# Kernel tuning notes

Hardware: AMD Instinct MI355X
Metric: run time of the kernel (lower is better)

## Reference

```python
import jax, jax.numpy as jnp
import numpy as np

B, D, R, E = 16384, 512, 64, 8

def setup_inputs() -> dict:
    key = jax.random.key(0)
    ks = jax.random.split(key, 8)
    return {
        "x0": jax.random.normal(ks[0], (B, D), jnp.float32),
        "x": jax.random.normal(ks[1], (B, D), jnp.float32),
        "U": jax.random.normal(ks[2], (E, D, R), jnp.float32) * 0.02,
        "V": jax.random.normal(ks[3], (E, R, D), jnp.float32) * 0.02,
        "C": jax.random.normal(ks[4], (E, R, R), jnp.float32) * 0.02,
        "b": jnp.zeros((E, D), jnp.float32),
        "Wg": jax.random.normal(ks[5], (E, D), jnp.float32) * 0.02,
        "bg": jnp.zeros((E,), jnp.float32),
    }

def reference(x0, x, U, V, C, b, Wg, bg):
    # gate: softmax over experts
    g = jax.nn.softmax(x @ Wg.T + bg, axis=1)            # [B, E]
    # per-expert low-rank bilinear transform, batched over experts
    xv = jnp.einsum('bd,erd->ber', x, V)                 # x @ V[e].T
    xvc = jnp.einsum('ber,ers->bes', xv, C)              # xv @ C[e]
    proj = jnp.einsum('bes,eds->bed', xvc, U)            # xvc @ U[e].T
    # gated sum: sum_e g_e * (x0*proj_e + b_e + x)
    gproj = jnp.einsum('be,bed->bd', g, proj)
    out = x0 * gproj + g @ b + x * g.sum(axis=1, keepdims=True)
    return out
```

## Files before the change

### kernel.cpp

```cpp
#include <hip/hip_runtime.h>
#include <math.h>


typedef __bf16 bf16_t;
typedef __attribute__((ext_vector_type(8))) __bf16 bf16x8;
typedef __attribute__((ext_vector_type(4))) __bf16 bf16x4;
typedef __attribute__((ext_vector_type(4))) float  floatx4;

__global__ __launch_bounds__(256) void prep_kernel(
    const float* __restrict__ U, const float* __restrict__ V, const float* __restrict__ C,
    bf16_t* __restrict__ VCc, bf16_t* __restrict__ Ut) {
  int tid = blockIdx.x * 256 + threadIdx.x;
  if (tid < 512 * 512) {
    int n = tid >> 9, d = tid & 511;
    int e = n >> 6, s = n & 63;
    const float* Vp = V + (size_t)e * 64 * 512 + d;
    const float* Cp = C + (size_t)e * 64 * 64 + s;
    float acc = 0.f;
#pragma unroll 8
    for (int r = 0; r < 64; ++r) acc += Vp[(size_t)r * 512] * Cp[r * 64];
    VCc[tid] = (bf16_t)acc;
  } else {
    int i2 = tid - 512 * 512;
    int d = i2 >> 9, n = i2 & 511;
    int e = n >> 6, s = n & 63;
    Ut[i2] = (bf16_t)U[((size_t)e * 512 + d) * 64 + s];
  }
}

__global__ __launch_bounds__(256) void gate_kernel(
    const float* __restrict__ x, const float* __restrict__ Wg, const float* __restrict__ bg,
    bf16_t* __restrict__ xbf, float* __restrict__ g) {
  int wave = threadIdx.x >> 6, lane = threadIdx.x & 63;
  int row = blockIdx.x * 4 + wave;
  const float4* xr = (const float4*)(x + (size_t)row * 512);
  float4 v0 = xr[lane];
  float4 v1 = xr[lane + 64];
  bf16x4* xb = (bf16x4*)(xbf + (size_t)row * 512);
  bf16x4 b0, b1;
  b0.x = (bf16_t)v0.x; b0.y = (bf16_t)v0.y; b0.z = (bf16_t)v0.z; b0.w = (bf16_t)v0.w;
  b1.x = (bf16_t)v1.x; b1.y = (bf16_t)v1.y; b1.z = (bf16_t)v1.z; b1.w = (bf16_t)v1.w;
  xb[lane] = b0;
  xb[lane + 64] = b1;
  float acc[8];
#pragma unroll
  for (int e = 0; e < 8; ++e) {
    const float4* wp = (const float4*)(Wg + (size_t)e * 512);
    float4 w0 = wp[lane], w1 = wp[lane + 64];
    acc[e] = v0.x * w0.x + v0.y * w0.y + v0.z * w0.z + v0.w * w0.w +
             v1.x * w1.x + v1.y * w1.y + v1.z * w1.z + v1.w * w1.w;
  }
#pragma unroll
  for (int e = 0; e < 8; ++e) {
#pragma unroll
    for (int off = 32; off > 0; off >>= 1) acc[e] += __shfl_xor(acc[e], off, 64);
  }
  float z[8], mx = -1e30f;
#pragma unroll
  for (int e = 0; e < 8; ++e) { z[e] = acc[e] + bg[e]; mx = fmaxf(mx, z[e]); }
  float s = 0.f;
#pragma unroll
  for (int e = 0; e < 8; ++e) { z[e] = __expf(z[e] - mx); s += z[e]; }
  float inv = 1.f / s;
  if (lane == 0) {
#pragma unroll
    for (int e = 0; e < 8; ++e) g[(size_t)row * 8 + e] = z[e] * inv;
  }
}

__device__ __forceinline__ void gemm_stream(
    const bf16_t* __restrict__ A, const bf16_t* __restrict__ Bt,
    char* ldsB, int m0, int n0, int t, floatx4 acc[2][4]) {
  {
    const float4* src = (const float4*)(Bt + (size_t)n0 * 512);
#pragma unroll
    for (int i = 0; i < 16; ++i) {
      int G = i * 256 + t;
      int n = G >> 6, c = G & 63;
      *(float4*)(ldsB + n * 1024 + ((c ^ (n & 7)) << 4)) = src[G];
    }
  }
  __syncthreads();
  const int lane = t & 63, wave = t >> 6;
  const int lhi = lane >> 4, llo = lane & 15;
  const char* pA0 = (const char*)A + (size_t)(m0 + wave * 32 + llo) * 1024 + lhi * 16;
  const char* pA1 = pA0 + 16 * 1024;
  const char* pB = ldsB + llo * 1024;
  const int bsw = (llo & 7) << 4;
#pragma unroll 4
  for (int ks = 0; ks < 16; ++ks) {
    bf16x8 a0 = *(const bf16x8*)(pA0 + ks * 64);
    bf16x8 a1 = *(const bf16x8*)(pA1 + ks * 64);
    bf16x8 bf[4];
#pragma unroll
    for (int nf = 0; nf < 4; ++nf)
      bf[nf] = *(const bf16x8*)(pB + nf * 16 * 1024 + ((((ks * 4 + lhi) << 4) ^ bsw)));
#pragma unroll
    for (int nf = 0; nf < 4; ++nf) {
      acc[0][nf] = __builtin_amdgcn_mfma_f32_16x16x32_bf16(a0, bf[nf], acc[0][nf], 0, 0, 0);
      acc[1][nf] = __builtin_amdgcn_mfma_f32_16x16x32_bf16(a1, bf[nf], acc[1][nf], 0, 0, 0);
    }
  }
}

__global__ __launch_bounds__(256, 2) void gemm1_kernel(
    const bf16_t* __restrict__ xbf, const bf16_t* __restrict__ VCc,
    const float* __restrict__ g, bf16_t* __restrict__ T) {
  __shared__ char lds[65536];
  const int t = threadIdx.x;
  const int m0 = blockIdx.x * 128, n0 = blockIdx.y * 64;
  floatx4 acc[2][4];
#pragma unroll
  for (int i = 0; i < 2; ++i)
#pragma unroll
    for (int j = 0; j < 4; ++j) acc[i][j] = (floatx4){0.f, 0.f, 0.f, 0.f};
  gemm_stream(xbf, VCc, lds, m0, n0, t, acc);
  __syncthreads();
  float* gcol = (float*)lds;
  if (t < 128) gcol[t] = g[(size_t)(m0 + t) * 8 + (n0 >> 6)];
  __syncthreads();
  const int lane = t & 63, wave = t >> 6;
  const int lhi = lane >> 4, llo = lane & 15;
#pragma unroll
  for (int mf = 0; mf < 2; ++mf) {
#pragma unroll
    for (int r = 0; r < 4; ++r) {
      int rml = wave * 32 + mf * 16 + lhi * 4 + r;
      float gv = gcol[rml];
      size_t mrow = (size_t)(m0 + rml) * 512;
#pragma unroll
      for (int nf = 0; nf < 4; ++nf)
        T[mrow + n0 + nf * 16 + llo] = (bf16_t)(acc[mf][nf][r] * gv);
    }
  }
}

__global__ __launch_bounds__(256, 2) void gemm2_kernel(
    const bf16_t* __restrict__ T, const bf16_t* __restrict__ Ut,
    const float* __restrict__ g, const float* __restrict__ bvec,
    const float* __restrict__ x0, const float* __restrict__ x,
    float* __restrict__ out) {
  __shared__ char lds[65536];
  const int t = threadIdx.x;
  const int m0 = blockIdx.x * 128, n0 = blockIdx.y * 64;
  floatx4 acc[2][4];
#pragma unroll
  for (int i = 0; i < 2; ++i)
#pragma unroll
    for (int j = 0; j < 4; ++j) acc[i][j] = (floatx4){0.f, 0.f, 0.f, 0.f};
  gemm_stream(T, Ut, lds, m0, n0, t, acc);
  __syncthreads();
  float* ldsG = (float*)lds;
  float* ldsBv = (float*)(lds + 4096);
  ((float4*)ldsG)[t] = ((const float4*)(g + (size_t)m0 * 8))[t];
  if (t < 128)
    ((float4*)ldsBv)[t] = ((const float4*)bvec)[(t >> 4) * 128 + (n0 >> 2) + (t & 15)];
  __syncthreads();
  const int lane = t & 63, wave = t >> 6;
  const int lhi = lane >> 4, llo = lane & 15;
  float bb[4][8];
#pragma unroll
  for (int nf = 0; nf < 4; ++nf) {
    int nl = nf * 16 + llo;
#pragma unroll
    for (int e = 0; e < 8; ++e) bb[nf][e] = ldsBv[e * 64 + nl];
  }
#pragma unroll
  for (int mf = 0; mf < 2; ++mf) {
#pragma unroll
    for (int r = 0; r < 4; ++r) {
      int rml = wave * 32 + mf * 16 + lhi * 4 + r;
      float4 ga = ((const float4*)ldsG)[rml * 2];
      float4 gb2 = ((const float4*)ldsG)[rml * 2 + 1];
      float g8[8] = {ga.x, ga.y, ga.z, ga.w, gb2.x, gb2.y, gb2.z, gb2.w};
      float gsum = g8[0] + g8[1] + g8[2] + g8[3] + g8[4] + g8[5] + g8[6] + g8[7];
      size_t mrow = (size_t)(m0 + rml) * 512;
#pragma unroll
      for (int nf = 0; nf < 4; ++nf) {
        int n = n0 + nf * 16 + llo;
        float bias = 0.f;
#pragma unroll
        for (int e = 0; e < 8; ++e) bias += g8[e] * bb[nf][e];
        size_t idx = mrow + n;
        out[idx] = x0[idx] * acc[mf][nf][r] + bias + x[idx] * gsum;
      }
    }
  }
}

extern "C" void kernel_launch(void* const* d_in, const int* in_sizes, int n_in,
                              void* d_out, int out_size, void* d_ws, size_t ws_size,
                              hipStream_t stream) {
  const float* x0 = (const float*)d_in[0];
  const float* x  = (const float*)d_in[1];
  const float* U  = (const float*)d_in[2];
  const float* V  = (const float*)d_in[3];
  const float* C  = (const float*)d_in[4];
  const float* bv = (const float*)d_in[5];
  const float* Wg = (const float*)d_in[6];
  const float* bg = (const float*)d_in[7];
  float* out = (float*)d_out;

  char* ws = (char*)d_ws;
  bf16_t* xbf = (bf16_t*)(ws);
  bf16_t* T   = (bf16_t*)(ws + 16777216);
  bf16_t* VCc = (bf16_t*)(ws + 33554432);
  bf16_t* Ut  = (bf16_t*)(ws + 34078720);
  float*  g   = (float*)(ws + 34603008);

  prep_kernel<<<2048, 256, 0, stream>>>(U, V, C, VCc, Ut);
  gate_kernel<<<4096, 256, 0, stream>>>(x, Wg, bg, xbf, g);
  gemm1_kernel<<<dim3(128, 8), 256, 0, stream>>>(xbf, VCc, g, T);
  gemm2_kernel<<<dim3(128, 8), 256, 0, stream>>>(T, Ut, g, bv, x0, x, out);
}
```

Baseline: 179.4 us.

## Read B fragments directly from global memory instead of staging in LDS

```diff
diff --git a/kernel.cpp b/kernel.cpp
--- a/kernel.cpp
+++ b/kernel.cpp
@@ -70,23 +70,12 @@
 
 __device__ __forceinline__ void gemm_stream(
     const bf16_t* __restrict__ A, const bf16_t* __restrict__ Bt,
-    char* ldsB, int m0, int n0, int t, floatx4 acc[2][4]) {
-  {
-    const float4* src = (const float4*)(Bt + (size_t)n0 * 512);
-#pragma unroll
-    for (int i = 0; i < 16; ++i) {
-      int G = i * 256 + t;
-      int n = G >> 6, c = G & 63;
-      *(float4*)(ldsB + n * 1024 + ((c ^ (n & 7)) << 4)) = src[G];
-    }
-  }
-  __syncthreads();
+    int m0, int n0, int t, floatx4 acc[2][4]) {
   const int lane = t & 63, wave = t >> 6;
   const int lhi = lane >> 4, llo = lane & 15;
   const char* pA0 = (const char*)A + (size_t)(m0 + wave * 32 + llo) * 1024 + lhi * 16;
   const char* pA1 = pA0 + 16 * 1024;
-  const char* pB = ldsB + llo * 1024;
-  const int bsw = (llo & 7) << 4;
+  const char* pB  = (const char*)Bt + (size_t)(n0 + llo) * 1024 + lhi * 16;
 #pragma unroll 4
   for (int ks = 0; ks < 16; ++ks) {
     bf16x8 a0 = *(const bf16x8*)(pA0 + ks * 64);
@@ -94,7 +83,7 @@
     bf16x8 bf[4];
 #pragma unroll
     for (int nf = 0; nf < 4; ++nf)
-      bf[nf] = *(const bf16x8*)(pB + nf * 16 * 1024 + ((((ks * 4 + lhi) << 4) ^ bsw)));
+      bf[nf] = *(const bf16x8*)(pB + (size_t)nf * 16 * 1024 + ks * 64);
 #pragma unroll
     for (int nf = 0; nf < 4; ++nf) {
       acc[0][nf] = __builtin_amdgcn_mfma_f32_16x16x32_bf16(a0, bf[nf], acc[0][nf], 0, 0, 0);
@@ -103,10 +92,10 @@
   }
 }
 
-__global__ __launch_bounds__(256, 2) void gemm1_kernel(
+__global__ __launch_bounds__(256, 4) void gemm1_kernel(
     const bf16_t* __restrict__ xbf, const bf16_t* __restrict__ VCc,
     const float* __restrict__ g, bf16_t* __restrict__ T) {
-  __shared__ char lds[65536];
+  __shared__ float gcol[128];
   const int t = threadIdx.x;
   const int m0 = blockIdx.x * 128, n0 = blockIdx.y * 64;
   floatx4 acc[2][4];
@@ -114,10 +103,8 @@
   for (int i = 0; i < 2; ++i)
 #pragma unroll
     for (int j = 0; j < 4; ++j) acc[i][j] = (floatx4){0.f, 0.f, 0.f, 0.f};
-  gemm_stream(xbf, VCc, lds, m0, n0, t, acc);
-  __syncthreads();
-  float* gcol = (float*)lds;
   if (t < 128) gcol[t] = g[(size_t)(m0 + t) * 8 + (n0 >> 6)];
+  gemm_stream(xbf, VCc, m0, n0, t, acc);
   __syncthreads();
   const int lane = t & 63, wave = t >> 6;
   const int lhi = lane >> 4, llo = lane & 15;
@@ -135,12 +122,13 @@
   }
 }
 
-__global__ __launch_bounds__(256, 2) void gemm2_kernel(
+__global__ __launch_bounds__(256, 4) void gemm2_kernel(
     const bf16_t* __restrict__ T, const bf16_t* __restrict__ Ut,
     const float* __restrict__ g, const float* __restrict__ bvec,
     const float* __restrict__ x0, const float* __restrict__ x,
     float* __restrict__ out) {
-  __shared__ char lds[65536];
+  __shared__ float ldsG[1024];
+  __shared__ float ldsBv[512];
   const int t = threadIdx.x;
   const int m0 = blockIdx.x * 128, n0 = blockIdx.y * 64;
   floatx4 acc[2][4];
@@ -148,13 +136,10 @@
   for (int i = 0; i < 2; ++i)
 #pragma unroll
     for (int j = 0; j < 4; ++j) acc[i][j] = (floatx4){0.f, 0.f, 0.f, 0.f};
-  gemm_stream(T, Ut, lds, m0, n0, t, acc);
-  __syncthreads();
-  float* ldsG = (float*)lds;
-  float* ldsBv = (float*)(lds + 4096);
   ((float4*)ldsG)[t] = ((const float4*)(g + (size_t)m0 * 8))[t];
   if (t < 128)
     ((float4*)ldsBv)[t] = ((const float4*)bvec)[(t >> 4) * 128 + (n0 >> 2) + (t & 15)];
+  gemm_stream(T, Ut, m0, n0, t, acc);
   __syncthreads();
   const int lane = t & 63, wave = t >> 6;
   const int lhi = lane >> 4, llo = lane & 15;
```

Result: slower. 229.0 us (+27.7%).
